# Performance work log

Hardware: AMD Instinct MI355X
Metric: run time of the kernel (lower is better)

## Reference

```python
import jax, jax.numpy as jnp
import numpy as np

N, C, H, W = 32, 128, 56, 56
K, KS = 256, 3
STRIDE, PAD = 1, 1


def setup_inputs() -> dict:
    key = jax.random.key(0)
    k1, k2, k3 = jax.random.split(key, 3)
    x = jax.random.normal(k1, (N, C, H, W), dtype=jnp.float32)
    stdv = 1.0 / np.sqrt(C * KS * KS)
    weight = jax.random.uniform(k2, (K, C, KS, KS), dtype=jnp.float32, minval=-stdv, maxval=stdv)
    bias = jax.random.uniform(k3, (K,), dtype=jnp.float32, minval=-stdv, maxval=stdv)
    return {"input": x, "weight": weight, "bias": bias}


def _binarize(t):
    # sign(t) * mean(|t|)  (XNOR-Net style scaled binarization)
    return jnp.sign(t) * jnp.mean(jnp.abs(t))


def reference(input, weight, bias):
    bx = _binarize(input)
    bw = _binarize(weight)
    out = jax.lax.conv_general_dilated(
        bx, bw,
        window_strides=(STRIDE, STRIDE),
        padding=[(PAD, PAD), (PAD, PAD)],
        dimension_numbers=("NCHW", "OIHW", "NCHW"),
    )
    return out + bias[None, :, None, None]
```

## Files before the change

### kernel.cpp

```cpp
#include <hip/hip_runtime.h>
#include <cstdint>

#define NB   32
#define CIN  128
#define HH   56
#define WW   56
#define KOUT 256
#define HWS  (HH*WW)
#define NHW  (NB*HWS)
#define PADH 58
#define XCNT ((float)(NB*CIN*HWS))
#define WCNT ((float)(KOUT*CIN*9))

__global__ __launch_bounds__(256) void init_kernel(uint4* __restrict__ xpad,
                                                   float* __restrict__ sums) {
    int idx = blockIdx.x * 256 + threadIdx.x;
    if (idx < 2) sums[idx] = 0.0f;
    int n = idx / 112, rem = idx - n * 112;
    int prow = (rem < 56) ? 0 : 57;
    int w = rem % 56;
    xpad[(n * PADH + prow) * WW + w] = make_uint4(0, 0, 0, 0);
}

__device__ __forceinline__ void block_reduce_add(float v, float* dst) {
    #pragma unroll
    for (int off = 32; off > 0; off >>= 1) v += __shfl_down(v, off);
    __shared__ float ws4[4];
    int lane = threadIdx.x & 63, wid = threadIdx.x >> 6;
    if (lane == 0) ws4[wid] = v;
    __syncthreads();
    if (threadIdx.x == 0) {
        float s = ws4[0];
        int nw = (blockDim.x + 63) >> 6;
        for (int i = 1; i < nw; i++) s += ws4[i];
        atomicAdd(dst, s);
    }
}

__global__ __launch_bounds__(256) void pack_x_kernel(const float* __restrict__ x,
                                                     uint32_t* __restrict__ xpadw,
                                                     float* __restrict__ sums) {
    int j   = blockIdx.x / (NHW / 256);
    int idx = (blockIdx.x - j * (NHW / 256)) * 256 + threadIdx.x;
    int n  = idx / HWS;
    int hw = idx - n * HWS;
    int h  = hw / WW;
    int w  = hw - h * WW;
    const float* p = x + (size_t)n * CIN * HWS + (size_t)(j * 32) * HWS + hw;
    float asum = 0.0f;
    uint32_t bits = 0;
    #pragma unroll
    for (int t = 0; t < 32; t++) {
        float v = p[(size_t)t * HWS];
        asum += fabsf(v);
        bits |= (v > 0.0f ? 1u : 0u) << t;
    }
    xpadw[(((n * PADH + h + 1) * WW + w) << 2) + j] = bits;
    block_reduce_add(asum, &sums[0]);
}

__global__ __launch_bounds__(256) void pack_w_kernel(const float* __restrict__ wgt,
                                                     uint32_t* __restrict__ wpackTw,
                                                     float* __restrict__ sums) {
    int k   = threadIdx.x;
    int tap = blockIdx.x >> 2;
    int j   = blockIdx.x & 3;
    const float* p = wgt + (size_t)k * CIN * 9 + (size_t)(j * 32) * 9 + tap;
    float asum = 0.0f;
    uint32_t bits = 0;
    #pragma unroll
    for (int t = 0; t < 32; t++) {
        float v = p[(size_t)t * 9];
        asum += fabsf(v);
        bits |= (v > 0.0f ? 1u : 0u) << t;
    }
    wpackTw[(tap * KOUT + k) * 4 + j] = bits;
    block_reduce_add(asum, &sums[1]);
}

__global__ __launch_bounds__(64, 4) void conv_kernel(const uint4* __restrict__ xpad,
                                                     const uint4* __restrict__ wpackT,
                                                     const float* __restrict__ sums,
                                                     const float* __restrict__ bias,
                                                     float* __restrict__ out) {
    __shared__ float sbuf[64 * 10];

    int l   = threadIdx.x;
    int bid = blockIdx.x;
    int kg  = bid & 3;
    int nh  = bid >> 2;
    int n   = nh / HH, h = nh - n * HH;
    int k   = kg * 64 + l;

    uint4 wq[9];
    #pragma unroll
    for (int t = 0; t < 9; t++) wq[t] = wpackT[t * KOUT + k];

    const uint4* P = xpad + (size_t)(n * PADH + h) * WW;

    uint4 xs[4][3];
#define PF(S, OFF) { xs[S][0] = PB[OFF]; xs[S][1] = PB[56 + (OFF)]; xs[S][2] = PB[112 + (OFF)]; }
    {
        const uint4* PB = P;
        PF(0, 0) PF(1, 1) PF(2, 2) PF(3, 3)
    }

    float scale = (sums[0] * (1.0f / XCNT)) * (sums[1] * (1.0f / WCNT));
    float m2s   = -2.0f * scale;
    float cbase = 1152.0f * scale + bias[k];

    int pw[9];
    #pragma unroll
    for (int t = 0; t < 9; t++)
        pw[t] = __popc(wq[t].x) + __popc(wq[t].y) + __popc(wq[t].z) + __popc(wq[t].w);
    int cs0 = pw[0] + pw[3] + pw[6];
    int cs2 = pw[2] + pw[5] + pw[8];
    int rterm = 0, cc0 = 0, cc2 = 0;
    if (h == 0)        { rterm = 2*(pw[0]+pw[1]+pw[2]) - 384; cc0 = 128 - 2*pw[0]; cc2 = 128 - 2*pw[2]; }
    else if (h == HH-1){ rterm = 2*(pw[6]+pw[7]+pw[8]) - 384; cc0 = 128 - 2*pw[6]; cc2 = 128 - 2*pw[8]; }
    float CB  = cbase + scale * (float)rterm;
    float F0  = CB + scale * (float)(2*cs0 - 384 + cc0);
    float F55 = CB + scale * (float)(2*cs2 - 384 + cc2);

    float* sb = &sbuf[l * 10];
    int fbase = (l >> 2) * 10 + (l & 3) * 2;
    float* o0 = out + ((size_t)(n * KOUT + kg * 64 + (l >> 2)) * HWS + h * WW + (l & 3) * 2);
    float* o1 = o0 + (size_t)16 * HWS;
    float* o2 = o1 + (size_t)16 * HWS;
    float* o3 = o2 + (size_t)16 * HWS;

#define T4(a, q, wt) a += __popc((q).x^(wt).x) + __popc((q).y^(wt).y) + __popc((q).z^(wt).z) + __popc((q).w^(wt).w);
#define FLUSH(C) { \
    *(float2*)(o0 + (C) * 8) = *(float2*)&sbuf[fbase];       \
    *(float2*)(o1 + (C) * 8) = *(float2*)&sbuf[fbase + 160]; \
    *(float2*)(o2 + (C) * 8) = *(float2*)&sbuf[fbase + 320]; \
    *(float2*)(o3 + (C) * 8) = *(float2*)&sbuf[fbase + 480]; \
}
#define CORE(J) \
    int a0 = 0, a1 = 0, a2 = 0; \
    T4(a0, xs[(J)&3][0], wq[0]) T4(a0, xs[((J)+1)&3][0], wq[1]) T4(a0, xs[((J)+2)&3][0], wq[2]) \
    T4(a1, xs[(J)&3][1], wq[3]) T4(a1, xs[((J)+1)&3][1], wq[4]) T4(a1, xs[((J)+2)&3][1], wq[5]) \
    T4(a2, xs[(J)&3][2], wq[6]) T4(a2, xs[((J)+1)&3][2], wq[7]) T4(a2, xs[((J)+2)&3][2], wq[8])
#define BODY(J)   { CORE(J) PF((J)&3, (J)+4) sb[((J)+1)&7] = fmaf(m2s, (float)(a0+a1+a2), CB); }
#define BODYNP(J) { CORE(J) sb[((J)+1)&7] = fmaf(m2s, (float)(a0+a1+a2), CB); }

    {
        int a0 = cs0, a1 = 0, a2 = 0;
        T4(a0, xs[0][0], wq[1]) T4(a0, xs[1][0], wq[2])
        T4(a1, xs[0][1], wq[4]) T4(a1, xs[1][1], wq[5])
        T4(a2, xs[0][2], wq[7]) T4(a2, xs[1][2], wq[8])
        sb[0] = fmaf(m2s, (float)(a0 + a1 + a2), F0);
    }

    {
        const uint4* PB = P;
        #pragma unroll 1
        for (int i = 0; i < 6; i++) {
            BODY(0) BODY(1) BODY(2) BODY(3) BODY(4) BODY(5)
            BODY(6)
            FLUSH(i)
            BODY(7)
            PB += 8;
        }
        BODY(0) BODY(1) BODY(2) BODY(3) BODYNP(4) BODYNP(5)
    }

    {
        int a0 = cs2, a1 = 0, a2 = 0;
        T4(a0, xs[2][0], wq[0]) T4(a0, xs[3][0], wq[1])
        T4(a1, xs[2][1], wq[3]) T4(a1, xs[3][1], wq[4])
        T4(a2, xs[2][2], wq[6]) T4(a2, xs[3][2], wq[7])
        sb[7] = fmaf(m2s, (float)(a0 + a1 + a2), F55);
        FLUSH(6)
    }
}

extern "C" void kernel_launch(void* const* d_in, const int* in_sizes, int n_in,
                              void* d_out, int out_size, void* d_ws, size_t ws_size,
                              hipStream_t stream) {
    const float* x    = (const float*)d_in[0];
    const float* wgt  = (const float*)d_in[1];
    const float* bias = (const float*)d_in[2];
    float* out = (float*)d_out;

    float* sums   = (float*)d_ws;
    uint4* xpad   = (uint4*)((char*)d_ws + 256);
    uint4* wpackT = (uint4*)((char*)d_ws + 256 + (size_t)NB * PADH * WW * 16);

    hipLaunchKernelGGL(init_kernel, dim3(14), dim3(256), 0, stream, xpad, sums);
    hipLaunchKernelGGL(pack_w_kernel, dim3(36), dim3(256), 0, stream, wgt, (uint32_t*)wpackT, sums);
    hipLaunchKernelGGL(pack_x_kernel, dim3(4 * NHW / 256), dim3(256), 0, stream, x, (uint32_t*)xpad, sums);
    hipLaunchKernelGGL(conv_kernel, dim3(NB * HH * 4), dim3(64), 0, stream, xpad, wpackT, sums, bias, out);
}
```

Baseline: 113.1 us.

## Merge output-channel groups into 256-thread blocks with inline-asm pipelined input loads

The conv kernel now runs one 256-thread block per (n,h) row, covering all four output-channel groups, where before there were four separate 64-thread blocks. The four waves in a block load the same input row, which could raise cache reuse. Input loads now go through inline global_load_dwordx4 asm with immediate offsets and explicit s_waitcnt vmcnt counts, so the prefetch depth is pinned by hand instead of left to the compiler's scheduling. The risk is that hand-written waitcnt counts are fragile: the compiler may reorder around the asm, and the larger block changes occupancy.

```diff
diff --git a/kernel.cpp b/kernel.cpp
--- a/kernel.cpp
+++ b/kernel.cpp
@@ -11,6 +11,8 @@
 #define PADH 58
 #define XCNT ((float)(NB*CIN*HWS))
 #define WCNT ((float)(KOUT*CIN*9))
+
+typedef uint32_t u32x4 __attribute__((ext_vector_type(4)));
 
 __global__ __launch_bounds__(256) void init_kernel(uint4* __restrict__ xpad,
                                                    float* __restrict__ sums) {
@@ -78,41 +80,33 @@
     block_reduce_add(asum, &sums[1]);
 }
 
-__global__ __launch_bounds__(64, 4) void conv_kernel(const uint4* __restrict__ xpad,
-                                                     const uint4* __restrict__ wpackT,
-                                                     const float* __restrict__ sums,
-                                                     const float* __restrict__ bias,
-                                                     float* __restrict__ out) {
-    __shared__ float sbuf[64 * 10];
-
-    int l   = threadIdx.x;
+__global__ __launch_bounds__(256, 4) void conv_kernel(const u32x4* __restrict__ xpad,
+                                                      const uint4* __restrict__ wpackT,
+                                                      const float* __restrict__ sums,
+                                                      const float* __restrict__ bias,
+                                                      float* __restrict__ out) {
+    __shared__ float sbuf[256 * 10];
+
+    int tid = threadIdx.x;
+    int l   = tid & 63, wid = tid >> 6;
     int bid = blockIdx.x;
-    int kg  = bid & 3;
-    int nh  = bid >> 2;
-    int n   = nh / HH, h = nh - n * HH;
-    int k   = kg * 64 + l;
-
-    uint4 wq[9];
-    #pragma unroll
-    for (int t = 0; t < 9; t++) wq[t] = wpackT[t * KOUT + k];
-
-    const uint4* P = xpad + (size_t)(n * PADH + h) * WW;
-
-    uint4 xs[4][3];
-#define PF(S, OFF) { xs[S][0] = PB[OFF]; xs[S][1] = PB[56 + (OFF)]; xs[S][2] = PB[112 + (OFF)]; }
-    {
-        const uint4* PB = P;
-        PF(0, 0) PF(1, 1) PF(2, 2) PF(3, 3)
+    int n   = bid / HH, h = bid - n * HH;
+
+    u32x4 wq[9];
+    #pragma unroll
+    for (int t = 0; t < 9; t++) {
+        uint4 q = wpackT[t * KOUT + tid];
+        wq[t] = (u32x4){q.x, q.y, q.z, q.w};
     }
 
     float scale = (sums[0] * (1.0f / XCNT)) * (sums[1] * (1.0f / WCNT));
     float m2s   = -2.0f * scale;
-    float cbase = 1152.0f * scale + bias[k];
+    float cbase = 1152.0f * scale + bias[tid];
 
     int pw[9];
     #pragma unroll
     for (int t = 0; t < 9; t++)
-        pw[t] = __popc(wq[t].x) + __popc(wq[t].y) + __popc(wq[t].z) + __popc(wq[t].w);
+        pw[t] = __popc(wq[t][0]) + __popc(wq[t][1]) + __popc(wq[t][2]) + __popc(wq[t][3]);
     int cs0 = pw[0] + pw[3] + pw[6];
     int cs2 = pw[2] + pw[5] + pw[8];
     int rterm = 0, cc0 = 0, cc2 = 0;
@@ -122,27 +116,43 @@
     float F0  = CB + scale * (float)(2*cs0 - 384 + cc0);
     float F55 = CB + scale * (float)(2*cs2 - 384 + cc2);
 
-    float* sb = &sbuf[l * 10];
-    int fbase = (l >> 2) * 10 + (l & 3) * 2;
-    float* o0 = out + ((size_t)(n * KOUT + kg * 64 + (l >> 2)) * HWS + h * WW + (l & 3) * 2);
-    float* o1 = o0 + (size_t)16 * HWS;
-    float* o2 = o1 + (size_t)16 * HWS;
-    float* o3 = o2 + (size_t)16 * HWS;
-
-#define T4(a, q, wt) a += __popc((q).x^(wt).x) + __popc((q).y^(wt).y) + __popc((q).z^(wt).z) + __popc((q).w^(wt).w);
-#define FLUSH(C) { \
-    *(float2*)(o0 + (C) * 8) = *(float2*)&sbuf[fbase];       \
-    *(float2*)(o1 + (C) * 8) = *(float2*)&sbuf[fbase + 160]; \
-    *(float2*)(o2 + (C) * 8) = *(float2*)&sbuf[fbase + 320]; \
-    *(float2*)(o3 + (C) * 8) = *(float2*)&sbuf[fbase + 480]; \
-}
+    const u32x4* R0 = xpad + (size_t)(n * PADH + h) * WW;
+    const u32x4* R1 = R0 + WW;
+    const u32x4* R2 = R1 + WW;
+
+    float* sb   = &sbuf[tid * 10];
+    int    fbase = (wid * 64 + (l >> 2)) * 10 + (l & 3) * 2;
+    float* o0   = out + ((size_t)(n * KOUT + wid * 64 + (l >> 2)) * HWS + h * WW + (l & 3) * 2);
+
+    u32x4 xs[4][3];
+
+#define GLD(dst, base, OFF) asm volatile("global_load_dwordx4 %0, %1, off offset:" OFF \
+                                         : "=v"(dst) : "v"(base));
+#define PF(S, OFF) { GLD(xs[S][0], R0, OFF) GLD(xs[S][1], R1, OFF) GLD(xs[S][2], R2, OFF) }
+#define WAITV(S, CNT) asm volatile("s_waitcnt vmcnt(" CNT ")" \
+                                   : "+v"(xs[S][0]), "+v"(xs[S][1]), "+v"(xs[S][2]));
+#define T4(a, q, wt) { u32x4 t_ = (q) ^ (wt); \
+    a += __popc(t_[0]) + __popc(t_[1]) + __popc(t_[2]) + __popc(t_[3]); }
 #define CORE(J) \
     int a0 = 0, a1 = 0, a2 = 0; \
     T4(a0, xs[(J)&3][0], wq[0]) T4(a0, xs[((J)+1)&3][0], wq[1]) T4(a0, xs[((J)+2)&3][0], wq[2]) \
     T4(a1, xs[(J)&3][1], wq[3]) T4(a1, xs[((J)+1)&3][1], wq[4]) T4(a1, xs[((J)+2)&3][1], wq[5]) \
     T4(a2, xs[(J)&3][2], wq[6]) T4(a2, xs[((J)+1)&3][2], wq[7]) T4(a2, xs[((J)+2)&3][2], wq[8])
-#define BODY(J)   { CORE(J) PF((J)&3, (J)+4) sb[((J)+1)&7] = fmaf(m2s, (float)(a0+a1+a2), CB); }
-#define BODYNP(J) { CORE(J) sb[((J)+1)&7] = fmaf(m2s, (float)(a0+a1+a2), CB); }
+#define BODY(J, OFF)    { WAITV(((J)+2)&3, "3") CORE(J) PF((J)&3, OFF) \
+                          sb[((J)+1)&7] = fmaf(m2s, (float)(a0+a1+a2), CB); }
+#define BODYNP(J, CNT)  { WAITV(((J)+2)&3, CNT) CORE(J) \
+                          sb[((J)+1)&7] = fmaf(m2s, (float)(a0+a1+a2), CB); }
+#define FLUSH { \
+    *(float2*)(o0)            = *(float2*)&sbuf[fbase]; \
+    *(float2*)(o0 + 16*HWS)   = *(float2*)&sbuf[fbase + 160]; \
+    *(float2*)(o0 + 32*HWS)   = *(float2*)&sbuf[fbase + 320]; \
+    *(float2*)(o0 + 48*HWS)   = *(float2*)&sbuf[fbase + 480]; \
+    o0 += 8; }
+
+    PF(0, "0") PF(1, "16") PF(2, "32") PF(3, "48")
+    asm volatile("s_waitcnt vmcnt(6)"
+                 : "+v"(xs[0][0]), "+v"(xs[0][1]), "+v"(xs[0][2]),
+                   "+v"(xs[1][0]), "+v"(xs[1][1]), "+v"(xs[1][2]));
 
     {
         int a0 = cs0, a1 = 0, a2 = 0;
@@ -152,18 +162,17 @@
         sb[0] = fmaf(m2s, (float)(a0 + a1 + a2), F0);
     }
 
-    {
-        const uint4* PB = P;
-        #pragma unroll 1
-        for (int i = 0; i < 6; i++) {
-            BODY(0) BODY(1) BODY(2) BODY(3) BODY(4) BODY(5)
-            BODY(6)
-            FLUSH(i)
-            BODY(7)
-            PB += 8;
-        }
-        BODY(0) BODY(1) BODY(2) BODY(3) BODYNP(4) BODYNP(5)
-    }
+    #pragma unroll 1
+    for (int i = 0; i < 6; i++) {
+        BODY(0, "64")  BODY(1, "80")  BODY(2, "96")  BODY(3, "112")
+        BODY(4, "128") BODY(5, "144") BODY(6, "160")
+        FLUSH
+        BODY(7, "176")
+        R0 += 8; R1 += 8; R2 += 8;
+    }
+
+    BODY(0, "64") BODY(1, "80") BODY(2, "96") BODY(3, "112")
+    BODYNP(4, "3") BODYNP(5, "0")
 
     {
         int a0 = cs2, a1 = 0, a2 = 0;
@@ -171,7 +180,7 @@
         T4(a1, xs[2][1], wq[3]) T4(a1, xs[3][1], wq[4])
         T4(a2, xs[2][2], wq[6]) T4(a2, xs[3][2], wq[7])
         sb[7] = fmaf(m2s, (float)(a0 + a1 + a2), F55);
-        FLUSH(6)
+        FLUSH
     }
 }
 
@@ -190,5 +199,6 @@
     hipLaunchKernelGGL(init_kernel, dim3(14), dim3(256), 0, stream, xpad, sums);
     hipLaunchKernelGGL(pack_w_kernel, dim3(36), dim3(256), 0, stream, wgt, (uint32_t*)wpackT, sums);
     hipLaunchKernelGGL(pack_x_kernel, dim3(4 * NHW / 256), dim3(256), 0, stream, x, (uint32_t*)xpad, sums);
-    hipLaunchKernelGGL(conv_kernel, dim3(NB * HH * 4), dim3(64), 0, stream, xpad, wpackT, sums, bias, out);
-}
+    hipLaunchKernelGGL(conv_kernel, dim3(NB * HH), dim3(256), 0, stream,
+                       (const u32x4*)xpad, wpackT, sums, bias, out);
+}
```

Measured after the change: 172.0 us. 1.52x slower.
